# Performance work log

Hardware: AMD Instinct MI355X
Metric: run time of the kernel (lower is better)

Reference implementation:

```python
import jax, jax.numpy as jnp
import numpy as np

B, T, N, IN_DIM, H, C, L, S, P = 64, 13, 325, 2, 64, 4, 2, 4, 12
NC = S * N  # combined temporal-graph node count per batch element


def _make_adj(rng, n, density=0.03):
    mask = rng.random((n, n)) < density
    return (mask * rng.random((n, n))).astype(np.float32)


def _combine(adj, s, forward):
    n = adj.shape[0]
    out = np.zeros((n * s, n * s), np.float32)
    for i in range(s):
        out[i * n:(i + 1) * n, i * n:(i + 1) * n] = adj
        if forward and i < s - 1:
            out[i * n:(i + 1) * n, (i + 1) * n:(i + 2) * n] = np.eye(n, dtype=np.float32)
    return out


def _checkpoints(s, t):
    mark, cp = s, []
    while mark < t:
        cp.append(mark)
        mark += s - 1
    if cp[-1] != t:
        cp.append(t)
    return cp


def setup_inputs():
    key = jax.random.key(0)
    ks = jax.random.split(key, 20)
    rng = np.random.default_rng(0)
    adj = _make_adj(rng, N)
    pea = _make_adj(rng, N)
    sc = 0.05
    inp = {
        'inputs': jax.random.normal(ks[0], (B, T, N, IN_DIM), jnp.float32),
        'adj_fwd': jnp.asarray(_combine(adj, S, True)),
        'adj_bwd': jnp.asarray(_combine(adj, S, False)),
        'pea_fwd': jnp.asarray(_combine(pea, S, True)),
        'pea_bwd': jnp.asarray(_combine(pea, S, False)),
        'w_in': sc * jax.random.normal(ks[1], (IN_DIM, H), jnp.float32),
        'b_in': jnp.zeros((H,), jnp.float32),
        'res_w': sc * jax.random.normal(ks[2], (S,), jnp.float32),
        'res_b': jnp.zeros((), jnp.float32),
        'gconv_w': sc * jax.random.normal(ks[3], (S,), jnp.float32),
        'gconv_b': jnp.zeros((), jnp.float32),
        'gate1_w': sc * jax.random.normal(ks[4], (H, H), jnp.float32),
        'gate1_b': jnp.zeros((H,), jnp.float32),
        'gate2_w': sc * jax.random.normal(ks[5], (H, H * C), jnp.float32),
        'gate2_b': jnp.zeros((H * C,), jnp.float32),
        'reduce_w': sc * jax.random.normal(ks[6], (C * H, H), jnp.float32),
        'reduce_b': jnp.zeros((H,), jnp.float32),
        'gcn_adj_w': sc * jax.random.normal(ks[7], (C, L, 2, H, H), jnp.float32),
        'gcn_adj_b': jnp.zeros((C, L, H), jnp.float32),
        'gcn_pea_w': sc * jax.random.normal(ks[8], (C, L, 2, H, H), jnp.float32),
        'gcn_pea_b': jnp.zeros((C, L, H), jnp.float32),
        'out_conv_w': sc * jax.random.normal(ks[9], (P,), jnp.float32),
        'out_conv_b': jnp.zeros((P,), jnp.float32),
        'out_lin_w': sc * jax.random.normal(ks[10], (H, 1), jnp.float32),
        'out_lin_b': jnp.zeros((1,), jnp.float32),
    }
    return inp


def _gcn_stack(feats, W, b, A_f, A_b, n_out):
    # feats [B, S*N, H]; W [L, 2, H, H]; weighted message passing over both supports
    h = feats
    for l in range(W.shape[0]):
        mf = jnp.einsum('nm,bmh->bnh', A_f, h)
        mb = jnp.einsum('nm,bmh->bnh', A_b, h)
        h = jax.nn.relu(mf @ W[l, 0] + mb @ W[l, 1] + b[l])
    return h[:, -n_out:, :]  # last snapshot's nodes -> [B, N, H]


def reference(inputs, adj_fwd, adj_bwd, pea_fwd, pea_bwd, w_in, b_in, res_w, res_b,
              gconv_w, gconv_b, gate1_w, gate1_b, gate2_w, gate2_b, reduce_w, reduce_b,
              gcn_adj_w, gcn_adj_b, gcn_pea_w, gcn_pea_b, out_conv_w, out_conv_b,
              out_lin_w, out_lin_b):
    b_, t_, n_, _ = inputs.shape
    h_ = w_in.shape[1]
    s_ = res_w.shape[0]
    c_ = gcn_adj_w.shape[0]
    x = inputs @ w_in + b_in  # [B, T, N, H]
    last = None
    left = 0
    for idx, right in enumerate(_checkpoints(s_, t_)):
        fs = x[:, left:right] if idx == 0 else jnp.concatenate([last, x[:, left:right]], axis=1)  # [B,S,N,H]
        gf = (jnp.einsum('s,bsnh->bnh', gconv_w, fs) + gconv_b).reshape(b_ * n_, h_)
        residual = jnp.einsum('s,bsnh->bnh', res_w, fs) + res_b  # [B,N,H]
        feats = fs.reshape(b_, s_ * n_, h_)
        ca = jnp.concatenate(
            [_gcn_stack(feats, gcn_adj_w[c], gcn_adj_b[c], adj_fwd, adj_bwd, n_) for c in range(c_)],
            axis=-1).reshape(b_ * n_, c_ * h_)
        cp = jnp.concatenate(
            [_gcn_stack(feats, gcn_pea_w[c], gcn_pea_b[c], pea_fwd, pea_bwd, n_) for c in range(c_)],
            axis=-1).reshape(b_ * n_, c_ * h_)
        gate = jax.nn.sigmoid(jax.nn.relu(gf @ gate1_w + gate1_b) @ gate2_w + gate2_b)
        gr = gate * ca + (1.0 - gate) * cp
        gr = (gr @ reduce_w + reduce_b).reshape(b_, n_, h_)
        cr = gr + residual
        # nn.LayerNorm([B, N, H], elementwise_affine=False): normalize over whole tensor
        mu = jnp.mean(cr)
        var = jnp.var(cr)
        last = ((cr - mu) * jax.lax.rsqrt(var + 1e-5))[:, None]  # [B,1,N,H]
        left = right
    # 1x1 conv 1->pred_len over channel dim, then linear H->1
    out = jax.nn.relu(out_conv_w.reshape(1, -1, 1, 1) * last + out_conv_b.reshape(1, -1, 1, 1))
    out = out @ out_lin_w + out_lin_b  # [B, pred_len, N, 1]
    return out
```

## Files before the change

kernel.cpp:

```cpp
#include <hip/hip_runtime.h>
#include <hip/hip_bf16.h>
#include <math.h>

#define B_    64
#define T_    13
#define N_    325
#define H_    64
#define C_    4
#define L_    2
#define S_    4
#define P_    12
#define KCP   4
#define M_    (B_*N_)
#define ADJLD 1300
#define NNZCAP 64
#define WPITCH 72
#define MTP   264
#define RTP   264
#define NBLK  1300

typedef short bfrag __attribute__((ext_vector_type(8)));
typedef float f32x4 __attribute__((ext_vector_type(4)));

__device__ __forceinline__ void fma4(float4& a, float s, float4 x) {
    a.x += s * x.x; a.y += s * x.y; a.z += s * x.z; a.w += s * x.w;
}
__device__ __forceinline__ ushort bf_rne(float f) {
    unsigned u = __float_as_uint(f);
    return (ushort)((u + 0x7fffu + ((u >> 16) & 1u)) >> 16);
}
__device__ __forceinline__ uint2 pack_bf4(float4 v) {
    unsigned a = __float_as_uint(v.x), b = __float_as_uint(v.y);
    unsigned c = __float_as_uint(v.z), d = __float_as_uint(v.w);
    a = (a + 0x7fffu + ((a >> 16) & 1u)) >> 16;
    b = (b + 0x7fffu + ((b >> 16) & 1u)) >> 16;
    c = (c + 0x7fffu + ((c >> 16) & 1u)) >> 16;
    d = (d + 0x7fffu + ((d >> 16) & 1u)) >> 16;
    return make_uint2(a | (b << 16), c | (d << 16));
}
__device__ __forceinline__ float4 unpack_bf4(uint2 p) {
    return make_float4(__uint_as_float(p.x << 16),
                       __uint_as_float(p.x & 0xffff0000u),
                       __uint_as_float(p.y << 16),
                       __uint_as_float(p.y & 0xffff0000u));
}

__global__ void k_build_sparse(const float* __restrict__ A,
                               int* __restrict__ cnt, int* __restrict__ cols,
                               float* __restrict__ vals) {
    int n    = blockIdx.x;
    int lane = threadIdx.x;
    const float* row = A + (size_t)n * ADJLD;
    int c = 0;
    for (int c0 = 0; c0 < 384; c0 += 64) {
        int col = c0 + lane;
        float v = (col < N_) ? row[col] : 0.f;
        unsigned long long m = __ballot(v != 0.f);
        int idx = c + __popcll(m & ((1ull << lane) - 1ull));
        if (v != 0.f && idx < NNZCAP) {
            cols[n * NNZCAP + idx] = col;
            vals[n * NNZCAP + idx] = v;
        }
        c += __popcll(m);
    }
    if (c + lane < NNZCAP) {
        cols[n * NNZCAP + c + lane] = 0;
        vals[n * NNZCAP + c + lane] = 0.f;
    }
    if (lane == 0) cnt[n] = (c < NNZCAP) ? c : NNZCAP;
}

__global__ void k_ginit(const float* __restrict__ inp,
                        const float* __restrict__ w_in, const float* __restrict__ b_in,
                        ushort* __restrict__ g_init4) {
    int idx = blockIdx.x * 256 + threadIdx.x;
    if (idx >= 4 * M_ * H_) return;
    int h  = idx & 63;
    int r  = idx >> 6;
    int it = r / M_;
    int m  = r - it * M_;
    int b  = m / N_, n = m % N_;
    int tt = 3 * it + 3;
    const float* ip = inp + ((size_t)(b * T_ + tt) * N_ + n) * 2;
    g_init4[idx] = bf_rne(ip[0] * w_in[h] + ip[1] * w_in[H_ + h] + b_in[h]);
}

__global__ void k_prep_w(const float* __restrict__ gadj_w,
                         const float* __restrict__ gpea_w,
                         ushort* __restrict__ WT) {
    int mat = blockIdx.x;
    int layer = mat >> 3, sm = mat & 7;
    int stack = sm >> 2, c = sm & 3;
    const float* w0 = (stack ? gpea_w : gadj_w) + (size_t)((c * L_ + layer) * 2) * 4096;
    const float* w1 = w0 + 4096;
    for (int i = 0; i < 16; ++i) {
        int e = threadIdx.x + i * 256;
        int k = e >> 6, n = e & 63;
        WT[((size_t)mat * 64 + n) * WPITCH + k] = bf_rne(w0[e] + w1[e]);
    }
}

__global__ void k_prep_rt(const float* __restrict__ reduce_w,
                          ushort* __restrict__ RT) {
    for (int i = 0; i < 64; ++i) {
        int e = threadIdx.x + i * 256;
        int k = e >> 6, n = e & 63;
        RT[(size_t)n * RTP + k] = bf_rne(reduce_w[e]);
    }
}

__global__ void k_prep_gate(const float* __restrict__ W1, const float* __restrict__ W2,
                            ushort* __restrict__ W1T, ushort* __restrict__ W2T) {
    int t = threadIdx.x;
    if (blockIdx.x == 0) {
        for (int i = 0; i < 16; ++i) {
            int e = t + i * 256;
            int k = e >> 6, n = e & 63;
            W1T[(size_t)n * WPITCH + k] = bf_rne(W1[e]);
        }
    } else {
        for (int i = 0; i < 64; ++i) {
            int e = t + i * 256;
            int k = e >> 8, n = e & 255;
            W2T[(size_t)n * WPITCH + k] = bf_rne(W2[e]);
        }
    }
}

__global__ __launch_bounds__(256, 4) void k_layer1(
    const int*   __restrict__ cnt,
    const int*   __restrict__ cols,
    const float* __restrict__ vals,
    const ushort* __restrict__ g_init4,
    int it0,
    const ushort* __restrict__ WT,
    const float* __restrict__ badj, const float* __restrict__ bpea,
    ushort* __restrict__ G1a4, ushort* __restrict__ G1p4)
{
    __shared__ __align__(16) ushort MaH[32 * WPITCH];
    __shared__ __align__(16) ushort MpH[32 * WPITCH];
    int t = threadIdx.x, lane = t & 63, w = t >> 6;
    int itk = blockIdx.x / 656;
    int lx  = blockIdx.x - itk * 656;
    int vb = (lx & 7) * 82 + (lx >> 3);
    if (vb >= 650) return;
    int m0 = vb * 32;
    const ushort* g_init = g_init4 + (size_t)(it0 + itk) * M_ * H_;
    ushort* G1a = G1a4 + (size_t)itk * M_ * 256;
    ushort* G1p = G1p4 + (size_t)itk * M_ * 256;
    int q = lane >> 4, ml = lane & 15;
    int colg = w * 16 + ml;

    {
        int cl = lane & 15, rr = lane >> 4;
        int mA = m0 + w * 8 + rr;
        int mB = mA + 4;
        int nA = mA % N_, nB = mB % N_;
        const ushort* gA = g_init + (size_t)(mA - nA) * H_ + cl * 4;
        const ushort* gB = g_init + (size_t)(mB - nB) * H_ + cl * 4;
        const int   *cA0 = cols + nA * NNZCAP,        *cB0 = cols + nB * NNZCAP;
        const float *vA0 = vals + nA * NNZCAP,        *vB0 = vals + nB * NNZCAP;
        const int   *cA1 = cols + (N_ + nA) * NNZCAP, *cB1 = cols + (N_ + nB) * NNZCAP;
        const float *vA1 = vals + (N_ + nA) * NNZCAP, *vB1 = vals + (N_ + nB) * NNZCAP;
        int jm = max(max(cnt[nA], cnt[nB]), max(cnt[N_ + nA], cnt[N_ + nB]));
        float4 aA0 = make_float4(0.f,0.f,0.f,0.f), aB0 = make_float4(0.f,0.f,0.f,0.f);
        float4 aA1 = make_float4(0.f,0.f,0.f,0.f), aB1 = make_float4(0.f,0.f,0.f,0.f);
        for (int j = 0; j < jm; j += 2) {
            fma4(aA0, vA0[j],   unpack_bf4(*(const uint2*)&gA[cA0[j]   * H_]));
            fma4(aA0, vA0[j+1], unpack_bf4(*(const uint2*)&gA[cA0[j+1] * H_]));
            fma4(aB0, vB0[j],   unpack_bf4(*(const uint2*)&gB[cB0[j]   * H_]));
            fma4(aB0, vB0[j+1], unpack_bf4(*(const uint2*)&gB[cB0[j+1] * H_]));
            fma4(aA1, vA1[j],   unpack_bf4(*(const uint2*)&gA[cA1[j]   * H_]));
            fma4(aA1, vA1[j+1], unpack_bf4(*(const uint2*)&gA[cA1[j+1] * H_]));
            fma4(aB1, vB1[j],   unpack_bf4(*(const uint2*)&gB[cB1[j]   * H_]));
            fma4(aB1, vB1[j+1], unpack_bf4(*(const uint2*)&gB[cB1[j+1] * H_]));
        }
        *(uint2*)&MaH[(w * 8 + rr) * WPITCH + cl * 4]     = pack_bf4(aA0);
        *(uint2*)&MaH[(w * 8 + 4 + rr) * WPITCH + cl * 4] = pack_bf4(aB0);
        *(uint2*)&MpH[(w * 8 + rr) * WPITCH + cl * 4]     = pack_bf4(aA1);
        *(uint2*)&MpH[(w * 8 + 4 + rr) * WPITCH + cl * 4] = pack_bf4(aB1);
    }
    __syncthreads();

    bfrag B0c = *(const bfrag*)&WT[(size_t)colg * WPITCH + q * 8];
    bfrag B1c = *(const bfrag*)&WT[(size_t)colg * WPITCH + 32 + q * 8];
    #pragma unroll
    for (int sc = 0; sc < 8; ++sc) {
        int stack = sc >> 2, c = sc & 3;
        bfrag B0n = B0c, B1n = B1c;
        if (sc < 7) {
            B0n = *(const bfrag*)&WT[((size_t)(sc + 1) * 64 + colg) * WPITCH + q * 8];
            B1n = *(const bfrag*)&WT[((size_t)(sc + 1) * 64 + colg) * WPITCH + 32 + q * 8];
        }
        const ushort* Msrc = stack ? MpH : MaH;
        float bv = (stack ? bpea : badj)[c * L_ * H_ + colg];
        ushort* Gout = stack ? G1p : G1a;
        #pragma unroll
        for (int r = 0; r < 2; ++r) {
            bfrag A0 = *(const bfrag*)&Msrc[(16 * r + ml) * WPITCH + q * 8];
            bfrag A1 = *(const bfrag*)&Msrc[(16 * r + ml) * WPITCH + 32 + q * 8];
            f32x4 acc = {0.f, 0.f, 0.f, 0.f};
            acc = __builtin_amdgcn_mfma_f32_16x16x32_bf16(A0, B0c, acc, 0, 0, 0);
            acc = __builtin_amdgcn_mfma_f32_16x16x32_bf16(A1, B1c, acc, 0, 0, 0);
            #pragma unroll
            for (int j = 0; j < 4; ++j) {
                float v = acc[j] + bv;
                v = v > 0.f ? v : 0.f;
                Gout[(size_t)(m0 + 16 * r + q * 4 + j) * 256 + c * 64 + colg] = bf_rne(v);
            }
        }
        B0c = B0n; B1c = B1n;
    }
}

__global__ __launch_bounds__(256, 4) void k_mix(
    const float* __restrict__ inp,
    const float* __restrict__ w_in, const float* __restrict__ b_in,
    const float* __restrict__ gconv_w, const float* __restrict__ gconv_b,
    const float* __restrict__ res_w,   const float* __restrict__ res_b,
    const float* __restrict__ cr_in, int it,
    const ushort* __restrict__ W1T, const float* __restrict__ b1,
    const ushort* __restrict__ W2T, const float* __restrict__ b2,
    const int*   __restrict__ cnt,
    const int*   __restrict__ cols,
    const float* __restrict__ vals,
    const ushort* __restrict__ G1a, const ushort* __restrict__ G1p,
    const ushort* __restrict__ WT,
    const float* __restrict__ badj, const float* __restrict__ bpea,
    const ushort* __restrict__ RT,
    const float* __restrict__ reduce_b,
    float* __restrict__ cr,
    const float* __restrict__ partials_in,
    float* __restrict__ partials)
{
    __shared__ __align__(16) ushort MtA[16 * MTP];
    __shared__ __align__(16) ushort MtP[16 * MTP];
    __shared__ __align__(16) ushort Gf[16 * WPITCH];
    __shared__ __align__(16) ushort Gr[16 * WPITCH];
    __shared__ float RES[16 * 68];
    __shared__ float red[8];
    int t = threadIdx.x, lane = t & 63, w = t >> 6;
    int vb = (blockIdx.x & 7) * 163 + (blockIdx.x >> 3);
    if (vb >= NBLK) return;
    int m0 = vb * 16;
    int q = lane >> 4, ml = lane & 15;
    int colg = w * 16 + ml;

    float mu = 0.f, rs = 0.f;
    if (it > 0) {
        float* REDS = (float*)MtA;
        float a = 0.f, b = 0.f;
        for (int i = t; i < NBLK; i += 256) { a += partials_in[i]; b += partials_in[NBLK + i]; }
        REDS[t] = a; REDS[256 + t] = b;
        __syncthreads();
        for (int off = 128; off > 0; off >>= 1) {
            if (t < off) { REDS[t] += REDS[t + off]; REDS[256 + t] += REDS[256 + t + off]; }
            __syncthreads();
        }
        const float inv = 1.f / (float)(M_ * H_);
        mu = REDS[0] * inv;
        float var = REDS[256] * inv - mu * mu;
        rs = rsqrtf(var + 1e-5f);
        __syncthreads();
    }

    {
        float wa = w_in[lane], wb = w_in[H_ + lane], bi = b_in[lane];
        float gw0 = gconv_w[0], gw1 = gconv_w[1], gw2 = gconv_w[2], gw3 = gconv_w[3];
        float rw0 = res_w[0],   rw1 = res_w[1],   rw2 = res_w[2],   rw3 = res_w[3];
        float gb = gconv_b[0],  rb = res_b[0];
        int t1 = (it == 0) ? 1 : (3 * it + 1);
        for (int i = 0; i < 4; ++i) {
            int r = i * 4 + w;
            int m = m0 + r;
            int b = m / N_, n = m % N_;
            const float* ipb = inp + ((size_t)b * T_ * N_ + n) * 2;
            float v0;
            if (it > 0) v0 = (cr_in[(size_t)m * H_ + lane] - mu) * rs;
            else        v0 = ipb[0] * wa + ipb[1] * wb + bi;
            const float* ip1 = ipb + (size_t)t1 * N_ * 2;
            const float* ip2 = ip1 + (size_t)N_ * 2;
            const float* ip3 = ip2 + (size_t)N_ * 2;
            float v1 = ip1[0] * wa + ip1[1] * wb + bi;
            float v2 = ip2[0] * wa + ip2[1] * wb + bi;
            float v3 = ip3[0] * wa + ip3[1] * wb + bi;
            Gf[r * WPITCH + lane] = bf_rne(gb + gw0 * v0 + gw1 * v1 + gw2 * v2 + gw3 * v3);
            RES[r * 68 + lane]    = rb + rw0 * v0 + rw1 * v1 + rw2 * v2 + rw3 * v3;
        }
    }
    __syncthreads();

    {
        bfrag A0 = *(const bfrag*)&Gf[ml * WPITCH + q * 8];
        bfrag A1 = *(const bfrag*)&Gf[ml * WPITCH + 32 + q * 8];
        bfrag B0 = *(const bfrag*)&W1T[(size_t)colg * WPITCH + q * 8];
        bfrag B1 = *(const bfrag*)&W1T[(size_t)colg * WPITCH + 32 + q * 8];
        f32x4 acc = {0.f, 0.f, 0.f, 0.f};
        acc = __builtin_amdgcn_mfma_f32_16x16x32_bf16(A0, B0, acc, 0, 0, 0);
        acc = __builtin_amdgcn_mfma_f32_16x16x32_bf16(A1, B1, acc, 0, 0, 0);
        float bb = b1[colg];
        #pragma unroll
        for (int j = 0; j < 4; ++j) {
            float v = acc[j] + bb;
            v = v > 0.f ? v : 0.f;
            Gr[(q * 4 + j) * WPITCH + colg] = bf_rne(v);
        }
    }
    __syncthreads();

    f32x4 gsv[4];
    {
        bfrag A0 = *(const bfrag*)&Gr[ml * WPITCH + q * 8];
        bfrag A1 = *(const bfrag*)&Gr[ml * WPITCH + 32 + q * 8];
        #pragma unroll
        for (int c = 0; c < 4; ++c) {
            bfrag B0 = *(const bfrag*)&W2T[(size_t)(c * 64 + colg) * WPITCH + q * 8];
            bfrag B1 = *(const bfrag*)&W2T[(size_t)(c * 64 + colg) * WPITCH + 32 + q * 8];
            f32x4 acc = {0.f, 0.f, 0.f, 0.f};
            acc = __builtin_amdgcn_mfma_f32_16x16x32_bf16(A0, B0, acc, 0, 0, 0);
            acc = __builtin_amdgcn_mfma_f32_16x16x32_bf16(A1, B1, acc, 0, 0, 0);
            float bb = b2[c * 64 + colg];
            #pragma unroll
            for (int j = 0; j < 4; ++j)
                gsv[c][j] = 1.f / (1.f + expf(-(acc[j] + bb)));
        }
    }

    for (int pp = 0; pp < 4; pp += 2) {
        int ma = m0 + w * 4 + pp, mb = ma + 1;
        int na = ma % N_, nb = mb % N_;
        const ushort* ga = G1a + (size_t)(ma - na) * 256 + lane * 4;
        const ushort* gb = G1a + (size_t)(mb - nb) * 256 + lane * 4;
        const ushort* pa = G1p + (size_t)(ma - na) * 256 + lane * 4;
        const ushort* pb = G1p + (size_t)(mb - nb) * 256 + lane * 4;
        const int   *cA0 = cols + na * NNZCAP,        *cB0 = cols + nb * NNZCAP;
        const float *vA0 = vals + na * NNZCAP,        *vB0 = vals + nb * NNZCAP;
        const int   *cA1 = cols + (N_ + na) * NNZCAP, *cB1 = cols + (N_ + nb) * NNZCAP;
        const float *vA1 = vals + (N_ + na) * NNZCAP, *vB1 = vals + (N_ + nb) * NNZCAP;
        int jm = max(max(cnt[na], cnt[nb]), max(cnt[N_ + na], cnt[N_ + nb]));
        float4 a0 = make_float4(0.f,0.f,0.f,0.f), a1 = make_float4(0.f,0.f,0.f,0.f);
        float4 p0 = make_float4(0.f,0.f,0.f,0.f), p1 = make_float4(0.f,0.f,0.f,0.f);
        for (int j = 0; j < jm; j += 2) {
            fma4(a0, vA0[j],   unpack_bf4(*(const uint2*)&ga[cA0[j]   * 256]));
            fma4(a0, vA0[j+1], unpack_bf4(*(const uint2*)&ga[cA0[j+1] * 256]));
            fma4(a1, vB0[j],   unpack_bf4(*(const uint2*)&gb[cB0[j]   * 256]));
            fma4(a1, vB0[j+1], unpack_bf4(*(const uint2*)&gb[cB0[j+1] * 256]));
            fma4(p0, vA1[j],   unpack_bf4(*(const uint2*)&pa[cA1[j]   * 256]));
            fma4(p0, vA1[j+1], unpack_bf4(*(const uint2*)&pa[cA1[j+1] * 256]));
            fma4(p1, vB1[j],   unpack_bf4(*(const uint2*)&pb[cB1[j]   * 256]));
            fma4(p1, vB1[j+1], unpack_bf4(*(const uint2*)&pb[cB1[j+1] * 256]));
        }
        int row0 = w * 4 + pp;
        *(uint2*)&MtA[row0 * MTP + lane * 4]       = pack_bf4(a0);
        *(uint2*)&MtA[(row0 + 1) * MTP + lane * 4] = pack_bf4(a1);
        *(uint2*)&MtP[row0 * MTP + lane * 4]       = pack_bf4(p0);
        *(uint2*)&MtP[(row0 + 1) * MTP + lane * 4] = pack_bf4(p1);
    }
    __syncthreads();

    const ushort* WT1 = WT + (size_t)8 * 64 * WPITCH;
    f32x4 res[4];
    bfrag B0c = *(const bfrag*)&WT1[(size_t)colg * WPITCH + q * 8];
    bfrag B1c = *(const bfrag*)&WT1[(size_t)colg * WPITCH + 32 + q * 8];
    #pragma unroll
    for (int sc = 0; sc < 8; ++sc) {
        int stack = sc >> 2, c = sc & 3;
        bfrag B0n = B0c, B1n = B1c;
        if (sc < 7) {
            B0n = *(const bfrag*)&WT1[((size_t)(sc + 1) * 64 + colg) * WPITCH + q * 8];
            B1n = *(const bfrag*)&WT1[((size_t)(sc + 1) * 64 + colg) * WPITCH + 32 + q * 8];
        }
        const ushort* Msrc = stack ? MtP : MtA;
        float bv = (stack ? bpea : badj)[(c * L_ + 1) * H_ + colg];
        bfrag A0 = *(const bfrag*)&Msrc[ml * MTP + c * 64 + q * 8];
        bfrag A1 = *(const bfrag*)&Msrc[ml * MTP + c * 64 + 32 + q * 8];
        f32x4 acc = {0.f, 0.f, 0.f, 0.f};
        acc = __builtin_amdgcn_mfma_f32_16x16x32_bf16(A0, B0c, acc, 0, 0, 0);
        acc = __builtin_amdgcn_mfma_f32_16x16x32_bf16(A1, B1c, acc, 0, 0, 0);
        #pragma unroll
        for (int j = 0; j < 4; ++j) {
            float v = acc[j] + bv;
            v = v > 0.f ? v : 0.f;
            if (stack == 0) res[c][j] = gsv[c][j] * v;
            else            res[c][j] += (1.f - gsv[c][j]) * v;
        }
        B0c = B0n; B1c = B1n;
    }

    bfrag RF[8];
    #pragma unroll
    for (int kc = 0; kc < 8; ++kc)
        RF[kc] = *(const bfrag*)&RT[(size_t)colg * RTP + kc * 32 + q * 8];
    f32x4 rv;
    #pragma unroll
    for (int j = 0; j < 4; ++j)
        rv[j] = RES[(q * 4 + j) * 68 + colg];

    __syncthreads();
    #pragma unroll
    for (int c = 0; c < 4; ++c)
        #pragma unroll
        for (int j = 0; j < 4; ++j)
            MtA[(q * 4 + j) * MTP + c * 64 + colg] = bf_rne(res[c][j]);
    __syncthreads();

    f32x4 racc = {0.f, 0.f, 0.f, 0.f};
    #pragma unroll
    for (int kc = 0; kc < 8; ++kc) {
        bfrag A0 = *(const bfrag*)&MtA[ml * MTP + kc * 32 + q * 8];
        racc = __builtin_amdgcn_mfma_f32_16x16x32_bf16(A0, RF[kc], racc, 0, 0, 0);
    }

    float bi = reduce_b[colg];
    float s = 0.f, s2 = 0.f;
    #pragma unroll
    for (int j = 0; j < 4; ++j) {
        int m = m0 + q * 4 + j;
        float v = racc[j] + bi + rv[j];
        cr[(size_t)m * 64 + colg] = v;
        s += v; s2 += v * v;
    }
    #pragma unroll
    for (int off = 32; off > 0; off >>= 1) {
        s  += __shfl_xor(s, off);
        s2 += __shfl_xor(s2, off);
    }
    if (lane == 0) { red[w] = s; red[4 + w] = s2; }
    __syncthreads();
    if (t == 0) partials[vb]        = red[0] + red[1] + red[2] + red[3];
    if (t == 1) partials[NBLK + vb] = red[4] + red[5] + red[6] + red[7];
}

__global__ __launch_bounds__(64) void k_out(
    const float* __restrict__ cr, const float* __restrict__ partials,
    const float* __restrict__ ocw, const float* __restrict__ ocb,
    const float* __restrict__ olw, const float* __restrict__ olb,
    float* __restrict__ out) {
    int t = threadIdx.x;
    float a = 0.f, b2s = 0.f;
    for (int i = t; i < NBLK; i += 64) { a += partials[i]; b2s += partials[NBLK + i]; }
    #pragma unroll
    for (int off = 32; off > 0; off >>= 1) {
        a   += __shfl_xor(a, off);
        b2s += __shfl_xor(b2s, off);
    }
    const float inv = 1.f / (float)(M_ * H_);
    float mu  = a * inv;
    float var = b2s * inv - mu * mu;
    float rs  = rsqrtf(var + 1e-5f);

    int m = blockIdx.x * 64 + t;
    int b = m / N_, n = m % N_;
    float cw[P_], cb[P_], acc[P_];
    #pragma unroll
    for (int p = 0; p < P_; ++p) { cw[p] = ocw[p]; cb[p] = ocb[p]; acc[p] = 0.f; }
    const float* lr = cr + (size_t)m * H_;
    for (int h4 = 0; h4 < 64; h4 += 4) {
        float4 lv4 = *(const float4*)&lr[h4];
        float4 wv4 = *(const float4*)&olw[h4];
        float lv[4] = {(lv4.x - mu) * rs, (lv4.y - mu) * rs,
                       (lv4.z - mu) * rs, (lv4.w - mu) * rs};
        float wv[4] = {wv4.x, wv4.y, wv4.z, wv4.w};
        #pragma unroll
        for (int e = 0; e < 4; ++e) {
            float lvv = lv[e], wvv = wv[e];
            #pragma unroll
            for (int p = 0; p < P_; ++p) {
                float u = cw[p] * lvv + cb[p];
                u = u > 0.f ? u : 0.f;
                acc[p] += u * wvv;
            }
        }
    }
    float ob = olb[0];
    #pragma unroll
    for (int p = 0; p < P_; ++p)
        out[(size_t)(b * P_ + p) * N_ + n] = acc[p] + ob;
}

extern "C" void kernel_launch(void* const* d_in, const int* in_sizes, int n_in,
                              void* d_out, int out_size, void* d_ws, size_t ws_size,
                              hipStream_t stream) {
    const float* inp      = (const float*)d_in[0];
    const float* adj_fwd  = (const float*)d_in[1];
    const float* pea_fwd  = (const float*)d_in[3];
    const float* w_in     = (const float*)d_in[5];
    const float* b_in     = (const float*)d_in[6];
    const float* res_w    = (const float*)d_in[7];
    const float* res_b    = (const float*)d_in[8];
    const float* gconv_w  = (const float*)d_in[9];
    const float* gconv_b  = (const float*)d_in[10];
    const float* gate1_w  = (const float*)d_in[11];
    const float* gate1_b  = (const float*)d_in[12];
    const float* gate2_w  = (const float*)d_in[13];
    const float* gate2_b  = (const float*)d_in[14];
    const float* reduce_w = (const float*)d_in[15];
    const float* reduce_b = (const float*)d_in[16];
    const float* gadj_w   = (const float*)d_in[17];
    const float* gadj_b   = (const float*)d_in[18];
    const float* gpea_w   = (const float*)d_in[19];
    const float* gpea_b   = (const float*)d_in[20];
    const float* ocw      = (const float*)d_in[21];
    const float* ocb      = (const float*)d_in[22];
    const float* olw      = (const float*)d_in[23];
    const float* olb      = (const float*)d_in[24];
    float* out = (float*)d_out;

    float* ws       = (float*)d_ws;
    float* cr       = ws;
    float* partials = cr + (size_t)M_ * H_;
    int*   scnt  = (int*)(partials + 2 * NBLK);
    int*   scols = scnt + 2 * N_;
    float* svals = (float*)(scols + 2 * N_ * NNZCAP);
    ushort* G1a4 = (ushort*)(svals + 2 * N_ * NNZCAP);
    ushort* G1p4 = G1a4 + 2 * (size_t)M_ * 256;
    ushort* g_init4 = G1p4 + 2 * (size_t)M_ * 256;
    ushort* WT   = g_init4 + 4 * (size_t)M_ * H_;
    WT = (ushort*)(((uintptr_t)WT + 15) & ~(uintptr_t)15);
    ushort* RT   = WT + 16 * 64 * WPITCH;
    ushort* W1T  = RT + 64 * RTP;
    ushort* W2T  = W1T + 64 * WPITCH;

    k_build_sparse<<<N_, 64, 0, stream>>>(adj_fwd, scnt,      scols,              svals);
    k_build_sparse<<<N_, 64, 0, stream>>>(pea_fwd, scnt + N_, scols + N_*NNZCAP,  svals + N_*NNZCAP);
    k_ginit<<<(4 * M_ * H_) / 256, 256, 0, stream>>>(inp, w_in, b_in, g_init4);
    k_prep_w<<<16, 256, 0, stream>>>(gadj_w, gpea_w, WT);
    k_prep_rt<<<1, 256, 0, stream>>>(reduce_w, RT);
    k_prep_gate<<<2, 256, 0, stream>>>(gate1_w, gate2_w, W1T, W2T);

    for (int half = 0; half < 2; ++half) {
        k_layer1<<<2 * 656, 256, 0, stream>>>(
            scnt, scols, svals, g_init4, half * 2,
            WT, gadj_b, gpea_b, G1a4, G1p4);
        for (int it = half * 2; it < half * 2 + 2; ++it) {
            int slot = it & 1;
            k_mix<<<1304, 256, 0, stream>>>(
                inp, w_in, b_in, gconv_w, gconv_b, res_w, res_b, cr, it,
                W1T, gate1_b, W2T, gate2_b,
                scnt, scols, svals,
                G1a4 + (size_t)slot * M_ * 256, G1p4 + (size_t)slot * M_ * 256,
                WT, gadj_b, gpea_b, RT, reduce_b, cr, partials, partials);
        }
    }

    k_out<<<N_, 64, 0, stream>>>(cr, partials, ocw, ocb, olw, olb, out);
}
```

Before: 474.6 us.

## Fuse setup kernels and overlap next-layer1 work inside mix launches

Merges the sparse-build, input-embedding and weight-prep kernels into one setup launch. Instead of two layer1 launches, it runs layer1 once for iteration 0 and embeds the layer1 blocks for iterations 2 and 3 as extra blocks in the mix launches of iterations 1 and 2, writing into the other double-buffer slot. The LayerNorm statistics reduction in mix now uses wave shuffles instead of a shared-memory tree, and layer1 preloads all weight fragments into registers. The aim is fewer launches and better GPU fill, at the cost of more register pressure and mixed block types competing within a launch.

```diff
diff --git a/kernel.cpp b/kernel.cpp
--- a/kernel.cpp
+++ b/kernel.cpp
@@ -18,6 +18,7 @@
 #define MTP   264
 #define RTP   264
 #define NBLK  1300
+#define MIXG  1304
 
 typedef short bfrag __attribute__((ext_vector_type(8)));
 typedef float f32x4 __attribute__((ext_vector_type(4)));
@@ -45,111 +46,104 @@
                        __uint_as_float(p.y & 0xffff0000u));
 }
 
-__global__ void k_build_sparse(const float* __restrict__ A,
-                               int* __restrict__ cnt, int* __restrict__ cols,
-                               float* __restrict__ vals) {
-    int n    = blockIdx.x;
-    int lane = threadIdx.x;
-    const float* row = A + (size_t)n * ADJLD;
-    int c = 0;
-    for (int c0 = 0; c0 < 384; c0 += 64) {
-        int col = c0 + lane;
-        float v = (col < N_) ? row[col] : 0.f;
-        unsigned long long m = __ballot(v != 0.f);
-        int idx = c + __popcll(m & ((1ull << lane) - 1ull));
-        if (v != 0.f && idx < NNZCAP) {
-            cols[n * NNZCAP + idx] = col;
-            vals[n * NNZCAP + idx] = v;
-        }
-        c += __popcll(m);
-    }
-    if (c + lane < NNZCAP) {
-        cols[n * NNZCAP + c + lane] = 0;
-        vals[n * NNZCAP + c + lane] = 0.f;
-    }
-    if (lane == 0) cnt[n] = (c < NNZCAP) ? c : NNZCAP;
-}
-
-__global__ void k_ginit(const float* __restrict__ inp,
-                        const float* __restrict__ w_in, const float* __restrict__ b_in,
-                        ushort* __restrict__ g_init4) {
-    int idx = blockIdx.x * 256 + threadIdx.x;
-    if (idx >= 4 * M_ * H_) return;
-    int h  = idx & 63;
-    int r  = idx >> 6;
-    int it = r / M_;
-    int m  = r - it * M_;
-    int b  = m / N_, n = m % N_;
-    int tt = 3 * it + 3;
-    const float* ip = inp + ((size_t)(b * T_ + tt) * N_ + n) * 2;
-    g_init4[idx] = bf_rne(ip[0] * w_in[h] + ip[1] * w_in[H_ + h] + b_in[h]);
-}
-
-__global__ void k_prep_w(const float* __restrict__ gadj_w,
-                         const float* __restrict__ gpea_w,
-                         ushort* __restrict__ WT) {
-    int mat = blockIdx.x;
-    int layer = mat >> 3, sm = mat & 7;
-    int stack = sm >> 2, c = sm & 3;
-    const float* w0 = (stack ? gpea_w : gadj_w) + (size_t)((c * L_ + layer) * 2) * 4096;
-    const float* w1 = w0 + 4096;
-    for (int i = 0; i < 16; ++i) {
-        int e = threadIdx.x + i * 256;
-        int k = e >> 6, n = e & 63;
-        WT[((size_t)mat * 64 + n) * WPITCH + k] = bf_rne(w0[e] + w1[e]);
-    }
-}
-
-__global__ void k_prep_rt(const float* __restrict__ reduce_w,
-                          ushort* __restrict__ RT) {
-    for (int i = 0; i < 64; ++i) {
-        int e = threadIdx.x + i * 256;
-        int k = e >> 6, n = e & 63;
-        RT[(size_t)n * RTP + k] = bf_rne(reduce_w[e]);
-    }
-}
-
-__global__ void k_prep_gate(const float* __restrict__ W1, const float* __restrict__ W2,
-                            ushort* __restrict__ W1T, ushort* __restrict__ W2T) {
-    int t = threadIdx.x;
-    if (blockIdx.x == 0) {
+__global__ void k_setup(
+    const float* __restrict__ adj_fwd, const float* __restrict__ pea_fwd,
+    const float* __restrict__ inp,
+    const float* __restrict__ w_in, const float* __restrict__ b_in,
+    const float* __restrict__ gadj_w, const float* __restrict__ gpea_w,
+    const float* __restrict__ reduce_w,
+    const float* __restrict__ gate1_w, const float* __restrict__ gate2_w,
+    int* __restrict__ cnt, int* __restrict__ cols, float* __restrict__ vals,
+    ushort* __restrict__ g_init4, ushort* __restrict__ WT,
+    ushort* __restrict__ RT, ushort* __restrict__ W1T, ushort* __restrict__ W2T)
+{
+    int bid = blockIdx.x, t = threadIdx.x;
+    if (bid >= 182) {
+        int idx = (bid - 182) * 256 + t;
+        if (idx >= 4 * M_ * H_) return;
+        int h  = idx & 63;
+        int r  = idx >> 6;
+        int it = r / M_;
+        int m  = r - it * M_;
+        int b  = m / N_, n = m % N_;
+        int tt = 3 * it + 3;
+        const float* ip = inp + ((size_t)(b * T_ + tt) * N_ + n) * 2;
+        g_init4[idx] = bf_rne(ip[0] * w_in[h] + ip[1] * w_in[H_ + h] + b_in[h]);
+    } else if (bid < 163) {
+        int lane = t & 63, w = t >> 6;
+        int row = bid * 4 + w;
+        if (row >= 2 * N_) return;
+        int mat = (row >= N_) ? 1 : 0;
+        int n   = row - mat * N_;
+        const float* A = mat ? pea_fwd : adj_fwd;
+        const float* rp = A + (size_t)n * ADJLD;
+        int* cw   = cols + (size_t)row * NNZCAP;
+        float* vw = vals + (size_t)row * NNZCAP;
+        int c = 0;
+        for (int c0 = 0; c0 < 384; c0 += 64) {
+            int col = c0 + lane;
+            float v = (col < N_) ? rp[col] : 0.f;
+            unsigned long long mmask = __ballot(v != 0.f);
+            int idx = c + __popcll(mmask & ((1ull << lane) - 1ull));
+            if (v != 0.f && idx < NNZCAP) { cw[idx] = col; vw[idx] = v; }
+            c += __popcll(mmask);
+        }
+        if (c + lane < NNZCAP) { cw[c + lane] = 0; vw[c + lane] = 0.f; }
+        if (lane == 0) cnt[row] = (c < NNZCAP) ? c : NNZCAP;
+    } else if (bid == 163) {
+        for (int i = 0; i < 64; ++i) {
+            int e = t + i * 256;
+            int k = e >> 6, n = e & 63;
+            RT[(size_t)n * RTP + k] = bf_rne(reduce_w[e]);
+        }
+    } else if (bid < 180) {
+        int mat = bid - 164;
+        int layer = mat >> 3, sm = mat & 7;
+        int stack = sm >> 2, c = sm & 3;
+        const float* w0 = (stack ? gpea_w : gadj_w) + (size_t)((c * L_ + layer) * 2) * 4096;
+        const float* w1 = w0 + 4096;
         for (int i = 0; i < 16; ++i) {
             int e = t + i * 256;
             int k = e >> 6, n = e & 63;
-            W1T[(size_t)n * WPITCH + k] = bf_rne(W1[e]);
+            WT[((size_t)mat * 64 + n) * WPITCH + k] = bf_rne(w0[e] + w1[e]);
+        }
+    } else if (bid == 180) {
+        for (int i = 0; i < 16; ++i) {
+            int e = t + i * 256;
+            int k = e >> 6, n = e & 63;
+            W1T[(size_t)n * WPITCH + k] = bf_rne(gate1_w[e]);
         }
     } else {
         for (int i = 0; i < 64; ++i) {
             int e = t + i * 256;
             int k = e >> 8, n = e & 255;
-            W2T[(size_t)n * WPITCH + k] = bf_rne(W2[e]);
-        }
-    }
-}
-
-__global__ __launch_bounds__(256, 4) void k_layer1(
+            W2T[(size_t)n * WPITCH + k] = bf_rne(gate2_w[e]);
+        }
+    }
+}
+
+__device__ __forceinline__ void l1_block(
+    int vb, int t,
     const int*   __restrict__ cnt,
     const int*   __restrict__ cols,
     const float* __restrict__ vals,
-    const ushort* __restrict__ g_init4,
-    int it0,
+    const ushort* __restrict__ g_init,
     const ushort* __restrict__ WT,
     const float* __restrict__ badj, const float* __restrict__ bpea,
-    ushort* __restrict__ G1a4, ushort* __restrict__ G1p4)
+    ushort* __restrict__ G1a, ushort* __restrict__ G1p,
+    ushort* MaH, ushort* MpH)
 {
-    __shared__ __align__(16) ushort MaH[32 * WPITCH];
-    __shared__ __align__(16) ushort MpH[32 * WPITCH];
-    int t = threadIdx.x, lane = t & 63, w = t >> 6;
-    int itk = blockIdx.x / 656;
-    int lx  = blockIdx.x - itk * 656;
-    int vb = (lx & 7) * 82 + (lx >> 3);
-    if (vb >= 650) return;
+    int lane = t & 63, w = t >> 6;
     int m0 = vb * 32;
-    const ushort* g_init = g_init4 + (size_t)(it0 + itk) * M_ * H_;
-    ushort* G1a = G1a4 + (size_t)itk * M_ * 256;
-    ushort* G1p = G1p4 + (size_t)itk * M_ * 256;
     int q = lane >> 4, ml = lane & 15;
     int colg = w * 16 + ml;
+
+    bfrag BF[8][2];
+    #pragma unroll
+    for (int mat = 0; mat < 8; ++mat)
+        #pragma unroll
+        for (int kc = 0; kc < 2; ++kc)
+            BF[mat][kc] = *(const bfrag*)&WT[((size_t)mat * 64 + colg) * WPITCH + kc * 32 + q * 8];
 
     {
         int cl = lane & 15, rr = lane >> 4;
@@ -182,16 +176,9 @@
     }
     __syncthreads();
 
-    bfrag B0c = *(const bfrag*)&WT[(size_t)colg * WPITCH + q * 8];
-    bfrag B1c = *(const bfrag*)&WT[(size_t)colg * WPITCH + 32 + q * 8];
     #pragma unroll
     for (int sc = 0; sc < 8; ++sc) {
         int stack = sc >> 2, c = sc & 3;
-        bfrag B0n = B0c, B1n = B1c;
-        if (sc < 7) {
-            B0n = *(const bfrag*)&WT[((size_t)(sc + 1) * 64 + colg) * WPITCH + q * 8];
-            B1n = *(const bfrag*)&WT[((size_t)(sc + 1) * 64 + colg) * WPITCH + 32 + q * 8];
-        }
         const ushort* Msrc = stack ? MpH : MaH;
         float bv = (stack ? bpea : badj)[c * L_ * H_ + colg];
         ushort* Gout = stack ? G1p : G1a;
@@ -200,8 +187,8 @@
             bfrag A0 = *(const bfrag*)&Msrc[(16 * r + ml) * WPITCH + q * 8];
             bfrag A1 = *(const bfrag*)&Msrc[(16 * r + ml) * WPITCH + 32 + q * 8];
             f32x4 acc = {0.f, 0.f, 0.f, 0.f};
-            acc = __builtin_amdgcn_mfma_f32_16x16x32_bf16(A0, B0c, acc, 0, 0, 0);
-            acc = __builtin_amdgcn_mfma_f32_16x16x32_bf16(A1, B1c, acc, 0, 0, 0);
+            acc = __builtin_amdgcn_mfma_f32_16x16x32_bf16(A0, BF[sc][0], acc, 0, 0, 0);
+            acc = __builtin_amdgcn_mfma_f32_16x16x32_bf16(A1, BF[sc][1], acc, 0, 0, 0);
             #pragma unroll
             for (int j = 0; j < 4; ++j) {
                 float v = acc[j] + bv;
@@ -209,8 +196,29 @@
                 Gout[(size_t)(m0 + 16 * r + q * 4 + j) * 256 + c * 64 + colg] = bf_rne(v);
             }
         }
-        B0c = B0n; B1c = B1n;
-    }
+    }
+}
+
+__global__ __launch_bounds__(256, 4) void k_layer1(
+    const int*   __restrict__ cnt,
+    const int*   __restrict__ cols,
+    const float* __restrict__ vals,
+    const ushort* __restrict__ g_init4,
+    int it0,
+    const ushort* __restrict__ WT,
+    const float* __restrict__ badj, const float* __restrict__ bpea,
+    ushort* __restrict__ G1a4, ushort* __restrict__ G1p4)
+{
+    __shared__ __align__(16) ushort MaH[32 * WPITCH];
+    __shared__ __align__(16) ushort MpH[32 * WPITCH];
+    int itk = blockIdx.x / 656;
+    int lx  = blockIdx.x - itk * 656;
+    int vb = (lx & 7) * 82 + (lx >> 3);
+    if (vb >= 650) return;
+    l1_block(vb, threadIdx.x, cnt, cols, vals,
+             g_init4 + (size_t)(it0 + itk) * M_ * H_, WT, badj, bpea,
+             G1a4 + (size_t)itk * M_ * 256, G1p4 + (size_t)itk * M_ * 256,
+             MaH, MpH);
 }
 
 __global__ __launch_bounds__(256, 4) void k_mix(
@@ -231,7 +239,9 @@
     const float* __restrict__ reduce_b,
     float* __restrict__ cr,
     const float* __restrict__ partials_in,
-    float* __restrict__ partials)
+    float* __restrict__ partials,
+    const ushort* __restrict__ g_init_l1,
+    ushort* __restrict__ G1a_wr, ushort* __restrict__ G1p_wr)
 {
     __shared__ __align__(16) ushort MtA[16 * MTP];
     __shared__ __align__(16) ushort MtP[16 * MTP];
@@ -240,6 +250,16 @@
     __shared__ float RES[16 * 68];
     __shared__ float red[8];
     int t = threadIdx.x, lane = t & 63, w = t >> 6;
+
+    if (blockIdx.x >= MIXG) {
+        int lx = blockIdx.x - MIXG;
+        int vb1 = (lx & 7) * 82 + (lx >> 3);
+        if (vb1 >= 650) return;
+        l1_block(vb1, t, cnt, cols, vals, g_init_l1, WT, badj, bpea,
+                 G1a_wr, G1p_wr, (ushort*)MtA, (ushort*)MtP);
+        return;
+    }
+
     int vb = (blockIdx.x & 7) * 163 + (blockIdx.x >> 3);
     if (vb >= NBLK) return;
     int m0 = vb * 16;
@@ -248,20 +268,21 @@
 
     float mu = 0.f, rs = 0.f;
     if (it > 0) {
-        float* REDS = (float*)MtA;
         float a = 0.f, b = 0.f;
         for (int i = t; i < NBLK; i += 256) { a += partials_in[i]; b += partials_in[NBLK + i]; }
-        REDS[t] = a; REDS[256 + t] = b;
+        #pragma unroll
+        for (int off = 32; off > 0; off >>= 1) {
+            a += __shfl_xor(a, off);
+            b += __shfl_xor(b, off);
+        }
+        if (lane == 0) { red[w] = a; red[4 + w] = b; }
         __syncthreads();
-        for (int off = 128; off > 0; off >>= 1) {
-            if (t < off) { REDS[t] += REDS[t + off]; REDS[256 + t] += REDS[256 + t + off]; }
-            __syncthreads();
-        }
+        a = red[0] + red[1] + red[2] + red[3];
+        b = red[4] + red[5] + red[6] + red[7];
         const float inv = 1.f / (float)(M_ * H_);
-        mu = REDS[0] * inv;
-        float var = REDS[256] * inv - mu * mu;
+        mu = a * inv;
+        float var = b * inv - mu * mu;
         rs = rsqrtf(var + 1e-5f);
-        __syncthreads();
     }
 
     {
@@ -521,26 +542,26 @@
     ushort* W1T  = RT + 64 * RTP;
     ushort* W2T  = W1T + 64 * WPITCH;
 
-    k_build_sparse<<<N_, 64, 0, stream>>>(adj_fwd, scnt,      scols,              svals);
-    k_build_sparse<<<N_, 64, 0, stream>>>(pea_fwd, scnt + N_, scols + N_*NNZCAP,  svals + N_*NNZCAP);
-    k_ginit<<<(4 * M_ * H_) / 256, 256, 0, stream>>>(inp, w_in, b_in, g_init4);
-    k_prep_w<<<16, 256, 0, stream>>>(gadj_w, gpea_w, WT);
-    k_prep_rt<<<1, 256, 0, stream>>>(reduce_w, RT);
-    k_prep_gate<<<2, 256, 0, stream>>>(gate1_w, gate2_w, W1T, W2T);
-
-    for (int half = 0; half < 2; ++half) {
-        k_layer1<<<2 * 656, 256, 0, stream>>>(
-            scnt, scols, svals, g_init4, half * 2,
-            WT, gadj_b, gpea_b, G1a4, G1p4);
-        for (int it = half * 2; it < half * 2 + 2; ++it) {
-            int slot = it & 1;
-            k_mix<<<1304, 256, 0, stream>>>(
-                inp, w_in, b_in, gconv_w, gconv_b, res_w, res_b, cr, it,
-                W1T, gate1_b, W2T, gate2_b,
-                scnt, scols, svals,
-                G1a4 + (size_t)slot * M_ * 256, G1p4 + (size_t)slot * M_ * 256,
-                WT, gadj_b, gpea_b, RT, reduce_b, cr, partials, partials);
-        }
+    k_setup<<<182 + (4 * M_ * H_) / 256, 256, 0, stream>>>(
+        adj_fwd, pea_fwd, inp, w_in, b_in, gadj_w, gpea_w, reduce_w,
+        gate1_w, gate2_w, scnt, scols, svals, g_init4, WT, RT, W1T, W2T);
+
+    k_layer1<<<1312, 256, 0, stream>>>(
+        scnt, scols, svals, g_init4, 0, WT, gadj_b, gpea_b, G1a4, G1p4);
+
+    for (int it = 0; it < 4; ++it) {
+        int slot = it & 1;
+        int embed = (it == 1 || it == 2);
+        int grid  = MIXG + (embed ? 656 : 0);
+        int wrsl  = (it + 1) & 1;
+        k_mix<<<grid, 256, 0, stream>>>(
+            inp, w_in, b_in, gconv_w, gconv_b, res_w, res_b, cr, it,
+            W1T, gate1_b, W2T, gate2_b,
+            scnt, scols, svals,
+            G1a4 + (size_t)slot * M_ * 256, G1p4 + (size_t)slot * M_ * 256,
+            WT, gadj_b, gpea_b, RT, reduce_b, cr, partials, partials,
+            g_init4 + (size_t)(it + 1) * M_ * H_,
+            G1a4 + (size_t)wrsl * M_ * 256, G1p4 + (size_t)wrsl * M_ * 256);
     }
 
     k_out<<<N_, 64, 0, stream>>>(cr, partials, ocw, ocb, olw, olb, out);
```

Measured after the change: 449.7 us. -5.2%, faster.
